# Performance work log

Hardware: AMD Instinct MI355X
Metric: run time of the kernel (lower is better)

Reference implementation:

```python
import jax, jax.numpy as jnp
import numpy as np

D_MODEL = 768
D_FF = 2048
NUM_EXPERTS = 8
TOP_K = 2


def setup_inputs() -> dict:
    key = jax.random.key(0)
    ks = jax.random.split(key, 5)
    s_in = 1.0 / np.sqrt(D_MODEL)
    s_ff = 1.0 / np.sqrt(D_FF)
    x = jax.random.normal(ks[0], (2, 1024, D_MODEL), dtype=jnp.float32)
    gate_w = jax.random.normal(ks[1], (D_MODEL, NUM_EXPERTS), dtype=jnp.float32) * s_in
    w_gate = jax.random.normal(ks[2], (NUM_EXPERTS, D_MODEL, D_FF), dtype=jnp.float32) * s_in
    w_up = jax.random.normal(ks[3], (NUM_EXPERTS, D_MODEL, D_FF), dtype=jnp.float32) * s_in
    w_down = jax.random.normal(ks[4], (NUM_EXPERTS, D_FF, D_MODEL), dtype=jnp.float32) * s_ff
    return {"x": x, "gate_w": gate_w, "w_gate": w_gate, "w_up": w_up, "w_down": w_down}


def reference(x, gate_w, w_gate, w_up, w_down):
    B, S, D = x.shape
    xf = x.reshape(-1, D)  # [T, D]

    # Router (eval mode: no noise)
    logits = xf @ gate_w                      # [T, E]
    gates = jax.nn.softmax(logits, axis=-1)
    top_g, top_i = jax.lax.top_k(gates, TOP_K)             # [T, K]
    top_g = top_g / jnp.sum(top_g, axis=-1, keepdims=True)

    # combine weights: [T, E] = sum_k gate_k * onehot(idx_k)
    combine = jnp.sum(
        jax.nn.one_hot(top_i, NUM_EXPERTS, dtype=xf.dtype) * top_g[..., None], axis=1
    )

    # SwiGLU experts computed densely, masked/weighted by combine
    g = jnp.einsum("td,edf->etf", xf, w_gate)  # [E, T, F]
    u = jnp.einsum("td,edf->etf", xf, w_up)
    h = jax.nn.silu(g) * u
    eo = jnp.einsum("etf,efd->etd", h, w_down)  # [E, T, D]
    out = jnp.einsum("te,etd->td", combine, eo)  # [T, D]

    load_balancing_loss = jnp.asarray(0.0, dtype=xf.dtype)  # eval mode
    return out.reshape(B, S, D), load_balancing_loss
```

## Files before the change

### kernel.cpp

```cpp
#include <hip/hip_runtime.h>
#include <stdint.h>

typedef __attribute__((ext_vector_type(8))) short short8;
typedef __attribute__((ext_vector_type(4))) float f32x4;
typedef unsigned int u32;
typedef unsigned short u16;

#define T_TOK 2048
#define DMODEL 768
#define DFF 2048
#define NEXP 8

#define BKP 40
#define WSTR 20

#define M_CNT 0
#define M_CUR 8
#define M_OFF 16

#define G1_GRID 640
#define G1_PERX 80
#define G2_GRID 432
#define G2_PERX 54

#define PREP_WT 9216
#define PREP_RT (PREP_WT + 512)
#define PREP_ZO (PREP_RT + 1536)

__device__ __forceinline__ float b2f(u16 u) {
  union { u32 i; float f; } v; v.i = ((u32)u) << 16; return v.f;
}
__device__ __forceinline__ u16 f2b(float f) {
  union { float f; u32 i; } v; v.f = f;
  return (u16)((v.i + 0x7fffu + ((v.i >> 16) & 1u)) >> 16);
}
__device__ __forceinline__ u32 pack2(float lo, float hi) {
  return (u32)f2b(lo) | ((u32)f2b(hi) << 16);
}
__device__ __forceinline__ uint4 cvt8(float4 a, float4 b) {
  uint4 r; r.x = pack2(a.x, a.y); r.y = pack2(a.z, a.w);
  r.z = pack2(b.x, b.y); r.w = pack2(b.z, b.w); return r;
}
__device__ __forceinline__ void gl16(const u16* g, u16* l) {
  __builtin_amdgcn_global_load_lds((const __attribute__((address_space(1))) void*)g,
                                   (__attribute__((address_space(3))) void*)l, 16, 0, 0);
}

__global__ __launch_bounds__(256) void k_prep(
    const float* __restrict__ wg, const float* __restrict__ wu, const float* __restrict__ wd,
    const float* __restrict__ x, const float* __restrict__ gw,
    u16* __restrict__ WgB, u16* __restrict__ WuB, u16* __restrict__ WdB,
    int* __restrict__ t2e, float* __restrict__ t2w, u16* __restrict__ xb,
    float* __restrict__ out) {
  __shared__ float T[32][136];
  int bid = blockIdx.x;
  int tid = threadIdx.x;
  if (bid < PREP_WT) {
    const float* in; u16* outw; int K, N, nx, ky, e, b;
    if (bid < 3072) { in = wg; outw = WgB; K = 768; N = 2048; b = bid; }
    else if (bid < 6144) { in = wu; outw = WuB; K = 768; N = 2048; b = bid - 3072; }
    else { in = wd; outw = WdB; K = 2048; N = 768; b = bid - 6144; }
    if (K == 768) {
      nx = b & 15; int r = b >> 4;
      e = (int)(((unsigned)r * 43691u) >> 20);
      ky = r - e * 24;
    } else {
      int q = (int)(((unsigned)b * 43691u) >> 18);
      nx = b - q * 6; ky = q & 63; e = q >> 6;
    }
    const float* ip = in + (size_t)e * K * N + (size_t)(ky * 32) * N + nx * 128;
    int kr = tid >> 3, nc = (tid & 7) * 16;
    const float* rp = ip + (size_t)kr * N + nc;
    float4 v0 = *(const float4*)(rp);
    float4 v1 = *(const float4*)(rp + 4);
    float4 v2 = *(const float4*)(rp + 8);
    float4 v3 = *(const float4*)(rp + 12);
    *(float4*)&T[kr][nc] = v0;
    *(float4*)&T[kr][nc + 4] = v1;
    *(float4*)&T[kr][nc + 8] = v2;
    *(float4*)&T[kr][nc + 12] = v3;
    __syncthreads();
    int nr = tid >> 1, kh = (tid & 1) * 16;
    float v[16];
#pragma unroll
    for (int j = 0; j < 16; ++j) v[j] = T[kh + j][nr];
    uint4 o0, o1;
    o0.x = pack2(v[0], v[1]);  o0.y = pack2(v[2], v[3]);
    o0.z = pack2(v[4], v[5]);  o0.w = pack2(v[6], v[7]);
    o1.x = pack2(v[8], v[9]);  o1.y = pack2(v[10], v[11]);
    o1.z = pack2(v[12], v[13]); o1.w = pack2(v[14], v[15]);
    int NB = N >> 7, KB = K >> 5;
    u16* op = outw + ((size_t)(e * NB + nx) * KB + ky) * 4096 + nr * 32 + kh;
    *(uint4*)op = o0;
    *(uint4*)(op + 8) = o1;
  } else if (bid < PREP_RT) {
    int lane = tid & 63;
    int t = (bid - PREP_WT) * 4 + (tid >> 6);
    const float* xr = x + (size_t)t * DMODEL;
    u16* xbr = xb + (size_t)t * DMODEL;
    float acc[8];
#pragma unroll
    for (int e = 0; e < 8; ++e) acc[e] = 0.f;
#pragma unroll
    for (int i = 0; i < 12; ++i) {
      int d = lane + (i << 6);
      float xd = xr[d];
      xbr[d] = f2b(xd);
      float4 g0 = *(const float4*)(gw + d * 8);
      float4 g1 = *(const float4*)(gw + d * 8 + 4);
      acc[0] += xd * g0.x; acc[1] += xd * g0.y;
      acc[2] += xd * g0.z; acc[3] += xd * g0.w;
      acc[4] += xd * g1.x; acc[5] += xd * g1.y;
      acc[6] += xd * g1.z; acc[7] += xd * g1.w;
    }
#pragma unroll
    for (int s = 32; s >= 1; s >>= 1) {
#pragma unroll
      for (int e = 0; e < 8; ++e) acc[e] += __shfl_xor(acc[e], s);
    }
    if (lane == 0) {
      int i0 = 0;
#pragma unroll
      for (int e = 1; e < 8; ++e) if (acc[e] > acc[i0]) i0 = e;
      int i1 = (i0 == 0) ? 1 : 0;
#pragma unroll
      for (int e = 0; e < 8; ++e) if (e != i0 && acc[e] > acc[i1]) i1 = e;
      float w0 = 1.f / (1.f + __expf(acc[i1] - acc[i0]));
      t2e[2 * t] = i0; t2e[2 * t + 1] = i1;
      t2w[2 * t] = w0; t2w[2 * t + 1] = 1.f - w0;
    }
  } else {
    int zid = bid - PREP_RT;
    float4 z = (float4){0.f, 0.f, 0.f, 0.f};
    *(float4*)(out + (size_t)(zid * 256 + tid) * 4) = z;
  }
}

__global__ __launch_bounds__(1024) void k_scansc(
    const int* __restrict__ t2e, const float* __restrict__ t2w, int* __restrict__ meta,
    int* __restrict__ tok_of_row, int* __restrict__ slot_of, float* __restrict__ w_of_row,
    float* __restrict__ outp) {
  __shared__ int cnt[8], cur[8];
  int tid = threadIdx.x;
  if (tid < 8) cnt[tid] = 0;
  __syncthreads();
  int e0a[2], e1a[2];
#pragma unroll
  for (int j = 0; j < 2; ++j) {
    int t = tid + j * 1024;
    e0a[j] = t2e[2 * t]; e1a[j] = t2e[2 * t + 1];
    atomicAdd(&cnt[e0a[j]], 1); atomicAdd(&cnt[e1a[j]], 1);
  }
  __syncthreads();
  if (tid == 0) {
    int r = 0;
#pragma unroll 1
    for (int e = 0; e < NEXP; ++e) {
      int c = cnt[e];
      meta[M_CNT + e] = c; meta[M_OFF + e] = r; cur[e] = r; r += c;
    }
    meta[M_OFF + NEXP] = r;
    outp[(size_t)T_TOK * DMODEL] = 0.f;
  }
  __syncthreads();
#pragma unroll
  for (int j = 0; j < 2; ++j) {
    int t = tid + j * 1024;
    int s0 = atomicAdd(&cur[e0a[j]], 1);
    tok_of_row[s0] = t; slot_of[2 * t] = s0; w_of_row[s0] = t2w[2 * t];
    int s1 = atomicAdd(&cur[e1a[j]], 1);
    tok_of_row[s1] = t; slot_of[2 * t + 1] = s1; w_of_row[s1] = t2w[2 * t + 1];
  }
}

__global__ __launch_bounds__(256, 3) void k_stage1b(
    const u16* __restrict__ Xb, const u16* __restrict__ WgB, const u16* __restrict__ WuB,
    const int* __restrict__ meta, const int* __restrict__ tok, u16* __restrict__ H) {
  __shared__ u16 Xs[2][4096];
  __shared__ u16 Wgs[2][4096];
  __shared__ u16 Wus[2][4096];
  int bid = blockIdx.x;
  int wid = (bid & 7) * G1_PERX + (bid >> 3);
  int e = 0, base = 0, Te = 0, off_e = 0, rows_e = 0;
#pragma unroll 1
  for (e = 0; e < NEXP; ++e) {
    off_e = meta[M_OFF + e];
    rows_e = meta[M_OFF + e + 1] - off_e;
    Te = (rows_e + 127) >> 7;
    int c = Te << 4;
    if (wid < base + c) break;
    base += c;
  }
  if (e == NEXP) return;
  int local = wid - base;
  int rb = local >> 4, fb = local & 15;
  int r0 = rb * 128;
  int rows_t = rows_e - r0; if (rows_t > 128) rows_t = 128;
  int f0 = fb * 128;
  int tid = threadIdx.x, lane = tid & 63, w = tid >> 6;
  int wr = w >> 1, wc = w & 1, q = lane >> 4, lm = lane & 15;

  int rsub = lane >> 2;
  int g4 = (lane & 3) ^ ((lane >> 3) & 3);
  int rA = w * 32 + rsub;
  int cA = (rA < rows_t) ? rA : (rows_t - 1);
  int cB = (rA + 16 < rows_t) ? (rA + 16) : (rows_t - 1);
  const u16* aG0 = Xb + (size_t)tok[off_e + r0 + cA] * DMODEL + g4 * 8;
  const u16* aG1 = Xb + (size_t)tok[off_e + r0 + cB] * DMODEL + g4 * 8;
  size_t cb = (size_t)((e * 16 + fb) * 24) * 4096 + w * 1024 + rsub * 32 + g4 * 8;
  const u16* gG = WgB + cb;
  const u16* uG = WuB + cb;

  int qx = (q ^ ((lm >> 1) & 3)) * 8;
  int aoff = (wr * 64 + lm) * 32 + qx;
  int boff = (wc * 64 + lm) * 32 + qx;

  f32x4 accg[4][4], accu[4][4];
#pragma unroll
  for (int i = 0; i < 4; ++i)
#pragma unroll
    for (int j = 0; j < 4; ++j) {
      accg[i][j] = (f32x4){0.f, 0.f, 0.f, 0.f};
      accu[i][j] = (f32x4){0.f, 0.f, 0.f, 0.f};
    }

  auto STG = [&](int b, int kko) {
    int ka = kko * 32;
    size_t kb = (size_t)kko * 4096;
    gl16(aG0 + ka, &Xs[b][w * 1024]);
    gl16(aG1 + ka, &Xs[b][w * 1024 + 512]);
    gl16(gG + kb, &Wgs[b][w * 1024]);
    gl16(gG + kb + 512, &Wgs[b][w * 1024 + 512]);
    gl16(uG + kb, &Wus[b][w * 1024]);
    gl16(uG + kb + 512, &Wus[b][w * 1024 + 512]);
  };
  auto CMP = [&](int b) {
    const u16* ap = &Xs[b][aoff];
    const u16* gp = &Wgs[b][boff];
    const u16* up = &Wus[b][boff];
    short8 af[4];
#pragma unroll
    for (int mt = 0; mt < 4; ++mt) af[mt] = *(const short8*)(ap + mt * 512);
#pragma unroll
    for (int nt = 0; nt < 4; ++nt) {
      short8 bg = *(const short8*)(gp + nt * 512);
      short8 bu = *(const short8*)(up + nt * 512);
#pragma unroll
      for (int mt = 0; mt < 4; ++mt) {
        accg[mt][nt] = __builtin_amdgcn_mfma_f32_16x16x32_bf16(af[mt], bg, accg[mt][nt], 0, 0, 0);
        accu[mt][nt] = __builtin_amdgcn_mfma_f32_16x16x32_bf16(af[mt], bu, accu[mt][nt], 0, 0, 0);
      }
    }
  };

  STG(0, 0);
  for (int kko = 0; kko < 23; ++kko) {
    STG((kko + 1) & 1, kko + 1);
    asm volatile("s_waitcnt vmcnt(6)" ::: "memory");
    __builtin_amdgcn_s_barrier();
    asm volatile("" ::: "memory");
    CMP(kko & 1);
    asm volatile("s_waitcnt lgkmcnt(0)" ::: "memory");
    __builtin_amdgcn_s_barrier();
    asm volatile("" ::: "memory");
  }
  asm volatile("s_waitcnt vmcnt(0)" ::: "memory");
  __builtin_amdgcn_s_barrier();
  asm volatile("" ::: "memory");
  CMP(1);

#pragma unroll
  for (int mt = 0; mt < 4; ++mt)
#pragma unroll
    for (int r = 0; r < 4; ++r) {
      int lrow = wr * 64 + mt * 16 + q * 4 + r;
      if (lrow < rows_t) {
        size_t rowbase = (size_t)(off_e + r0 + lrow) * DFF + f0 + wc * 64;
#pragma unroll
        for (int nt = 0; nt < 4; ++nt) {
          float g = accg[mt][nt][r], u = accu[mt][nt][r];
          float h = g / (1.f + __expf(-g)) * u;
          H[rowbase + nt * 16 + lm] = f2b(h);
        }
      }
    }
}

__global__ __launch_bounds__(256, 3) void k_stage2b(
    const u16* __restrict__ H, const u16* __restrict__ WdB,
    const int* __restrict__ meta, const int* __restrict__ tok,
    const float* __restrict__ wrow, float* __restrict__ out) {
  __shared__ u16 As[2][4096];
  __shared__ u16 Ws[2][8192];
  int bid = blockIdx.x;
  int wid = (bid & 7) * G2_PERX + (bid >> 3);
  int e = 0, base = 0, off_e = 0, rows_e = 0;
#pragma unroll 1
  for (e = 0; e < NEXP; ++e) {
    off_e = meta[M_OFF + e];
    rows_e = meta[M_OFF + e + 1] - off_e;
    int Tr = (rows_e + 63) >> 6;
    int c = Tr * 6;
    if (wid < base + c) break;
    base += c;
  }
  if (e == NEXP) return;
  int local = wid - base;
  int rb = (int)(((unsigned)local * 43691u) >> 18);
  int nb = local - rb * 6;
  int r0 = rb * 64;
  int rows_t = rows_e - r0; if (rows_t > 64) rows_t = 64;
  int n0 = nb * 128;
  int tid = threadIdx.x, lane = tid & 63, w = tid >> 6;
  int q = lane >> 4, lm = lane & 15;

  int rsub = lane >> 2;
  int g4 = (lane & 3) ^ ((lane >> 3) & 3);
  int rA = w * 16 + rsub;
  int cA = (rA < rows_t) ? rA : (rows_t - 1);
  const u16* aG = H + (size_t)(off_e + r0 + cA) * DFF + g4 * 8;
  size_t cb = (size_t)((e * 6 + nb) * 64) * 4096 + w * 1024 + rsub * 32 + g4 * 8;
  const u16* wG = WdB + cb;

  int qx = (q ^ ((lm >> 1) & 3)) * 8;
  int aoff = lm * 32 + qx;
  int boff = (w * 32 + lm) * 32 + qx;

  f32x4 acc[4][2];
#pragma unroll
  for (int i = 0; i < 4; ++i)
#pragma unroll
    for (int j = 0; j < 2; ++j) acc[i][j] = (f32x4){0.f, 0.f, 0.f, 0.f};

  auto STG = [&](int b, int kko) {
    int ka = kko * 64;
    size_t kb = (size_t)kko * 8192;
    gl16(aG + ka, &As[b][w * 512]);
    gl16(aG + ka + 32, &As[b][2048 + w * 512]);
    gl16(wG + kb, &Ws[b][w * 1024]);
    gl16(wG + kb + 512, &Ws[b][w * 1024 + 512]);
    gl16(wG + kb + 4096, &Ws[b][4096 + w * 1024]);
    gl16(wG + kb + 4608, &Ws[b][4096 + w * 1024 + 512]);
  };
  auto CMP = [&](int b) {
    const u16* ap = &As[b][aoff];
    const u16* bp = &Ws[b][boff];
#pragma unroll
    for (int s = 0; s < 2; ++s) {
      short8 af[4];
#pragma unroll
      for (int mt = 0; mt < 4; ++mt) af[mt] = *(const short8*)(ap + s * 2048 + mt * 512);
#pragma unroll
      for (int nt = 0; nt < 2; ++nt) {
        short8 bb = *(const short8*)(bp + s * 4096 + nt * 512);
#pragma unroll
        for (int mt = 0; mt < 4; ++mt)
          acc[mt][nt] = __builtin_amdgcn_mfma_f32_16x16x32_bf16(af[mt], bb, acc[mt][nt], 0, 0, 0);
      }
    }
  };

  STG(0, 0);
  for (int kko = 0; kko < 31; ++kko) {
    STG((kko + 1) & 1, kko + 1);
    asm volatile("s_waitcnt vmcnt(6)" ::: "memory");
    __builtin_amdgcn_s_barrier();
    asm volatile("" ::: "memory");
    CMP(kko & 1);
    asm volatile("s_waitcnt lgkmcnt(0)" ::: "memory");
    __builtin_amdgcn_s_barrier();
    asm volatile("" ::: "memory");
  }
  asm volatile("s_waitcnt vmcnt(0)" ::: "memory");
  __builtin_amdgcn_s_barrier();
  asm volatile("" ::: "memory");
  CMP(1);

#pragma unroll
  for (int mt = 0; mt < 4; ++mt)
#pragma unroll
    for (int r = 0; r < 4; ++r) {
      int lrow = mt * 16 + q * 4 + r;
      if (lrow < rows_t) {
        int row = off_e + r0 + lrow;
        int token = tok[row];
        float wgt = wrow[row];
        float* ob = out + (size_t)token * DMODEL + n0 + w * 32;
#pragma unroll
        for (int nt = 0; nt < 2; ++nt)
          atomicAdd(&ob[nt * 16 + lm], wgt * acc[mt][nt][r]);
      }
    }
}

__global__ __launch_bounds__(192) void k_combine(
    const float* __restrict__ Op, const int* __restrict__ slot_of,
    const float* __restrict__ t2w, float* __restrict__ out) {
  int t = blockIdx.x;
  int d4 = threadIdx.x << 2;
  int s0 = slot_of[2 * t], s1 = slot_of[2 * t + 1];
  float w0 = t2w[2 * t], w1 = t2w[2 * t + 1];
  float4 a = *(const float4*)&Op[(size_t)s0 * DMODEL + d4];
  float4 b = *(const float4*)&Op[(size_t)s1 * DMODEL + d4];
  float4 r;
  r.x = w0 * a.x + w1 * b.x;
  r.y = w0 * a.y + w1 * b.y;
  r.z = w0 * a.z + w1 * b.z;
  r.w = w0 * a.w + w1 * b.w;
  *(float4*)&out[(size_t)t * DMODEL + d4] = r;
}

__global__ __launch_bounds__(256) void k_router_fb(
    const float* __restrict__ x, const float* __restrict__ gw,
    int* __restrict__ t2e, float* __restrict__ t2w, u16* __restrict__ xb) {
  int lane = threadIdx.x & 63;
  int t = blockIdx.x * 4 + (threadIdx.x >> 6);
  const float* xr = x + (size_t)t * DMODEL;
  u16* xbr = xb + (size_t)t * DMODEL;
  float acc[8];
#pragma unroll
  for (int e = 0; e < 8; ++e) acc[e] = 0.f;
#pragma unroll
  for (int i = 0; i < 12; ++i) {
    int d = lane + (i << 6);
    float xd = xr[d];
    xbr[d] = f2b(xd);
    float4 g0 = *(const float4*)(gw + d * 8);
    float4 g1 = *(const float4*)(gw + d * 8 + 4);
    acc[0] += xd * g0.x; acc[1] += xd * g0.y;
    acc[2] += xd * g0.z; acc[3] += xd * g0.w;
    acc[4] += xd * g1.x; acc[5] += xd * g1.y;
    acc[6] += xd * g1.z; acc[7] += xd * g1.w;
  }
#pragma unroll
  for (int s = 32; s >= 1; s >>= 1) {
#pragma unroll
    for (int e = 0; e < 8; ++e) acc[e] += __shfl_xor(acc[e], s);
  }
  if (lane == 0) {
    int i0 = 0;
#pragma unroll
    for (int e = 1; e < 8; ++e) if (acc[e] > acc[i0]) i0 = e;
    int i1 = (i0 == 0) ? 1 : 0;
#pragma unroll
    for (int e = 0; e < 8; ++e) if (e != i0 && acc[e] > acc[i1]) i1 = e;
    float w0 = 1.f / (1.f + __expf(acc[i1] - acc[i0]));
    t2e[2 * t] = i0; t2e[2 * t + 1] = i1;
    t2w[2 * t] = w0; t2w[2 * t + 1] = 1.f - w0;
  }
}

__device__ __forceinline__ void wpack(u32* lds, int k2, int n8, uint4 a, uint4 b) {
  int idx = n8 * WSTR + k2;
  lds[idx + 0 * WSTR] = (a.x & 0xffffu) | (b.x << 16);
  lds[idx + 1 * WSTR] = (a.x >> 16) | (b.x & 0xffff0000u);
  lds[idx + 2 * WSTR] = (a.y & 0xffffu) | (b.y << 16);
  lds[idx + 3 * WSTR] = (a.y >> 16) | (b.y & 0xffff0000u);
  lds[idx + 4 * WSTR] = (a.z & 0xffffu) | (b.z << 16);
  lds[idx + 5 * WSTR] = (a.z >> 16) | (b.z & 0xffff0000u);
  lds[idx + 6 * WSTR] = (a.w & 0xffffu) | (b.w << 16);
  lds[idx + 7 * WSTR] = (a.w >> 16) | (b.w & 0xffff0000u);
}

__global__ __launch_bounds__(256) void k_stage1f(
    const float* __restrict__ xv, const float* __restrict__ wgv, const float* __restrict__ wuv,
    const int* __restrict__ meta, const int* __restrict__ tok, u16* __restrict__ H) {
  __shared__ u16 Xs[64 * 32];
  __shared__ u16 Wgs[128 * BKP];
  __shared__ u16 Wus[128 * BKP];
  int e = blockIdx.z;
  int off_e = meta[M_OFF + e];
  int rows_e = meta[M_OFF + e + 1] - off_e;
  int r0 = blockIdx.y * 64;
  if (r0 >= rows_e) return;
  int rows_t = rows_e - r0; if (rows_t > 64) rows_t = 64;
  int f0 = blockIdx.x * 128;
  int tid = threadIdx.x, lane = tid & 63, w = tid >> 6;
  int wr = w >> 1, wc = w & 1;
  int srow = (w << 4) + (lane >> 2);
  int trow = (srow < rows_t) ? tok[off_e + r0 + srow] : tok[off_e];
  int xcol = (lane & 3) << 3;
  u16* xl = &Xs[srow * 32 + xcol];
  int k2 = tid >> 4, n8 = (tid & 15) << 3;
  size_t wbase = (size_t)e * (DMODEL * DFF) + (size_t)(k2 << 1) * DFF + f0 + n8;
  f32x4 accg[2][4], accu[2][4];
#pragma unroll
  for (int i = 0; i < 2; ++i)
#pragma unroll
    for (int j = 0; j < 4; ++j) {
      accg[i][j] = (f32x4){0.f, 0.f, 0.f, 0.f};
      accu[i][j] = (f32x4){0.f, 0.f, 0.f, 0.f};
    }
  for (int kk = 0; kk < DMODEL / 32; ++kk) {
    int k0 = kk << 5;
    const float* xg = xv + (size_t)trow * DMODEL + xcol;
    const float* wgp = wgv + wbase;
    const float* wup = wuv + wbase;
    uint4 xa = cvt8(*(const float4*)(xg + k0), *(const float4*)(xg + k0 + 4));
    uint4 ga = cvt8(*(const float4*)(wgp + (size_t)k0 * DFF), *(const float4*)(wgp + (size_t)k0 * DFF + 4));
    uint4 gb = cvt8(*(const float4*)(wgp + (size_t)k0 * DFF + DFF), *(const float4*)(wgp + (size_t)k0 * DFF + DFF + 4));
    uint4 ua = cvt8(*(const float4*)(wup + (size_t)k0 * DFF), *(const float4*)(wup + (size_t)k0 * DFF + 4));
    uint4 ub = cvt8(*(const float4*)(wup + (size_t)k0 * DFF + DFF), *(const float4*)(wup + (size_t)k0 * DFF + DFF + 4));
    __syncthreads();
    *(uint4*)xl = xa;
    wpack((u32*)Wgs, k2, n8, ga, gb);
    wpack((u32*)Wus, k2, n8, ua, ub);
    __syncthreads();
    short8 af[2];
#pragma unroll
    for (int mt = 0; mt < 2; ++mt)
      af[mt] = *(const short8*)&Xs[((wr << 5) + (mt << 4) + (lane & 15)) * 32 + ((lane >> 4) << 3)];
#pragma unroll
    for (int nt = 0; nt < 4; ++nt) {
      int col = (wc << 6) + (nt << 4) + (lane & 15);
      short8 bg = *(const short8*)&Wgs[col * BKP + ((lane >> 4) << 3)];
      short8 bu = *(const short8*)&Wus[col * BKP + ((lane >> 4) << 3)];
#pragma unroll
      for (int mt = 0; mt < 2; ++mt) {
        accg[mt][nt] = __builtin_amdgcn_mfma_f32_16x16x32_bf16(af[mt], bg, accg[mt][nt], 0, 0, 0);
        accu[mt][nt] = __builtin_amdgcn_mfma_f32_16x16x32_bf16(af[mt], bu, accu[mt][nt], 0, 0, 0);
      }
    }
  }
  int q = lane >> 4, c = lane & 15;
#pragma unroll
  for (int mt = 0; mt < 2; ++mt)
#pragma unroll
    for (int r = 0; r < 4; ++r) {
      int lrow = (wr << 5) + (mt << 4) + (q << 2) + r;
      if (lrow < rows_t) {
        size_t rowbase = (size_t)(off_e + r0 + lrow) * DFF + f0 + (wc << 6);
#pragma unroll
        for (int nt = 0; nt < 4; ++nt) {
          float g = accg[mt][nt][r], u = accu[mt][nt][r];
          float h = g / (1.f + __expf(-g)) * u;
          H[rowbase + (nt << 4) + c] = f2b(h);
        }
      }
    }
}

__global__ __launch_bounds__(256) void k_stage2f(
    const u16* __restrict__ H, const float* __restrict__ wdv,
    const int* __restrict__ meta, float* __restrict__ Op) {
  __shared__ u16 As[64 * 32];
  __shared__ u16 Ws[128 * BKP];
  int e = blockIdx.z;
  int off_e = meta[M_OFF + e];
  int rows_e = meta[M_OFF + e + 1] - off_e;
  int r0 = blockIdx.y * 64;
  if (r0 >= rows_e) return;
  int rows_t = rows_e - r0; if (rows_t > 64) rows_t = 64;
  int n0 = blockIdx.x * 128;
  int tid = threadIdx.x, lane = tid & 63, w = tid >> 6;
  int wr = w >> 1, wc = w & 1;
  int srow = (w << 4) + (lane >> 2);
  int hrow = off_e + r0 + ((srow < rows_t) ? srow : 0);
  const u16* ag = H + (size_t)hrow * DFF + ((lane & 3) << 3);
  u16* al = &As[srow * 32 + ((lane & 3) << 3)];
  int k2 = tid >> 4, n8 = (tid & 15) << 3;
  size_t wbase = (size_t)e * (DFF * DMODEL) + (size_t)(k2 << 1) * DMODEL + n0 + n8;
  f32x4 acc[2][4];
#pragma unroll
  for (int i = 0; i < 2; ++i)
#pragma unroll
    for (int j = 0; j < 4; ++j) acc[i][j] = (f32x4){0.f, 0.f, 0.f, 0.f};
  for (int kk = 0; kk < DFF / 32; ++kk) {
    int k0 = kk << 5;
    uint4 xa = *(const uint4*)(ag + k0);
    const float* wdp = wdv + wbase;
    uint4 ga = cvt8(*(const float4*)(wdp + (size_t)k0 * DMODEL), *(const float4*)(wdp + (size_t)k0 * DMODEL + 4));
    uint4 gb = cvt8(*(const float4*)(wdp + (size_t)k0 * DMODEL + DMODEL), *(const float4*)(wdp + (size_t)k0 * DMODEL + DMODEL + 4));
    __syncthreads();
    *(uint4*)al = xa;
    wpack((u32*)Ws, k2, n8, ga, gb);
    __syncthreads();
    short8 af[2];
#pragma unroll
    for (int mt = 0; mt < 2; ++mt)
      af[mt] = *(const short8*)&As[((wr << 5) + (mt << 4) + (lane & 15)) * 32 + ((lane >> 4) << 3)];
#pragma unroll
    for (int nt = 0; nt < 4; ++nt) {
      int col = (wc << 6) + (nt << 4) + (lane & 15);
      short8 b = *(const short8*)&Ws[col * BKP + ((lane >> 4) << 3)];
#pragma unroll
      for (int mt = 0; mt < 2; ++mt)
        acc[mt][nt] = __builtin_amdgcn_mfma_f32_16x16x32_bf16(af[mt], b, acc[mt][nt], 0, 0, 0);
    }
  }
  int q = lane >> 4, c = lane & 15;
#pragma unroll
  for (int mt = 0; mt < 2; ++mt)
#pragma unroll
    for (int r = 0; r < 4; ++r) {
      int lrow = (wr << 5) + (mt << 4) + (q << 2) + r;
      if (lrow < rows_t) {
        size_t rowbase = (size_t)(off_e + r0 + lrow) * DMODEL + n0 + (wc << 6);
#pragma unroll
        for (int nt = 0; nt < 4; ++nt)
          Op[rowbase + (nt << 4) + c] = acc[mt][nt][r];
      }
    }
}

extern "C" void kernel_launch(void* const* d_in, const int* in_sizes, int n_in,
                              void* d_out, int out_size, void* d_ws, size_t ws_size,
                              hipStream_t stream) {
  const float* x  = (const float*)d_in[0];
  const float* gw = (const float*)d_in[1];
  const float* wg = (const float*)d_in[2];
  const float* wu = (const float*)d_in[3];
  const float* wd = (const float*)d_in[4];
  float* out = (float*)d_out;

  char* ws = (char*)d_ws;
  int* meta = (int*)ws;
  int* t2e        = (int*)(ws + 256);
  int* slot_of    = (int*)(ws + 16640);
  int* tok_of_row = (int*)(ws + 33024);
  float* t2w      = (float*)(ws + 49408);
  u16* Xb         = (u16*)(ws + 65792);

  const size_t NEED = 108069120;
  if (ws_size >= NEED) {
    u16* H         = (u16*)(ws + 3211520);
    float* w_of_row = (float*)(ws + 19988736);
    u16* WgB   = (u16*)(ws + 32571648);
    u16* WuB   = (u16*)(ws + 57737472);
    u16* WdB   = (u16*)(ws + 82903296);

    k_prep<<<PREP_ZO, 256, 0, stream>>>(wg, wu, wd, x, gw, WgB, WuB, WdB,
                                        t2e, t2w, Xb, out);
    k_scansc<<<1, 1024, 0, stream>>>(t2e, t2w, meta, tok_of_row, slot_of, w_of_row, out);
    k_stage1b<<<G1_GRID, 256, 0, stream>>>(Xb, WgB, WuB, meta, tok_of_row, H);
    k_stage2b<<<G2_GRID, 256, 0, stream>>>(H, WdB, meta, tok_of_row, w_of_row, out);
  } else {
    u16* H    = (u16*)(ws + 65792);
    float* Op = (float*)(ws + 65792 + 16777216);
    float* w_of_row = (float*)(ws + 65792 + 16777216 + 12582912);
    k_router_fb<<<T_TOK / 4, 256, 0, stream>>>(x, gw, t2e, t2w, Xb);
    k_scansc<<<1, 1024, 0, stream>>>(t2e, t2w, meta, tok_of_row, slot_of, w_of_row, out);
    dim3 g1(DFF / 128, T_TOK / 64, NEXP);
    k_stage1f<<<g1, 256, 0, stream>>>(x, wg, wu, meta, tok_of_row, H);
    dim3 g2(DMODEL / 128, T_TOK / 64, NEXP);
    k_stage2f<<<g2, 256, 0, stream>>>(H, wd, meta, Op);
    k_combine<<<T_TOK, 192, 0, stream>>>(Op, slot_of, t2w, out);
  }
}
```

Baseline: 261.9 us.

## Triple-buffer expert GEMM pipelines and batch weight conversion into fewer prep blocks

Both expert GEMM kernels move from double to triple buffering in shared memory, so two tiles stay in flight and the wait point loosens to vmcnt(12). Occupancy hints drop from 3 to 2 blocks per CU to make room for the larger LDS use. The prep kernel now converts eight k-tiles per block in a software-pipelined loop instead of launching one block per tile, and each zeroing block clears four times as much output. This cuts launch and block overhead and hides more memory latency, at the cost of occupancy and extra barriers.

```diff
diff --git a/kernel.cpp b/kernel.cpp
--- a/kernel.cpp
+++ b/kernel.cpp
@@ -23,9 +23,9 @@
 #define G2_GRID 432
 #define G2_PERX 54
 
-#define PREP_WT 9216
+#define PREP_WT 1152
 #define PREP_RT (PREP_WT + 512)
-#define PREP_ZO (PREP_RT + 1536)
+#define PREP_GRID (PREP_RT + 384)
 
 __device__ __forceinline__ float b2f(u16 u) {
   union { u32 i; float f; } v; v.i = ((u32)u) << 16; return v.f;
@@ -56,43 +56,59 @@
   int bid = blockIdx.x;
   int tid = threadIdx.x;
   if (bid < PREP_WT) {
-    const float* in; u16* outw; int K, N, nx, ky, e, b;
-    if (bid < 3072) { in = wg; outw = WgB; K = 768; N = 2048; b = bid; }
-    else if (bid < 6144) { in = wu; outw = WuB; K = 768; N = 2048; b = bid - 3072; }
-    else { in = wd; outw = WdB; K = 2048; N = 768; b = bid - 6144; }
+    const float* in; u16* outw; int K, N, b;
+    if (bid < 384) { in = wg; outw = WgB; K = 768; N = 2048; b = bid; }
+    else if (bid < 768) { in = wu; outw = WuB; K = 768; N = 2048; b = bid - 384; }
+    else { in = wd; outw = WdB; K = 2048; N = 768; b = bid - 768; }
+    int e, nx, ky0;
     if (K == 768) {
-      nx = b & 15; int r = b >> 4;
-      e = (int)(((unsigned)r * 43691u) >> 20);
-      ky = r - e * 24;
+      int t = (int)(((unsigned)b * 43691u) >> 17);
+      int kc = b - t * 3;
+      e = t >> 4; nx = t & 15; ky0 = kc * 8;
     } else {
-      int q = (int)(((unsigned)b * 43691u) >> 18);
-      nx = b - q * 6; ky = q & 63; e = q >> 6;
-    }
-    const float* ip = in + (size_t)e * K * N + (size_t)(ky * 32) * N + nx * 128;
+      int kc = b & 7; int t = b >> 3;
+      e = (int)(((unsigned)t * 43691u) >> 18);
+      nx = t - e * 6; ky0 = kc * 8;
+    }
     int kr = tid >> 3, nc = (tid & 7) * 16;
-    const float* rp = ip + (size_t)kr * N + nc;
-    float4 v0 = *(const float4*)(rp);
-    float4 v1 = *(const float4*)(rp + 4);
-    float4 v2 = *(const float4*)(rp + 8);
-    float4 v3 = *(const float4*)(rp + 12);
-    *(float4*)&T[kr][nc] = v0;
-    *(float4*)&T[kr][nc + 4] = v1;
-    *(float4*)&T[kr][nc + 8] = v2;
-    *(float4*)&T[kr][nc + 12] = v3;
-    __syncthreads();
     int nr = tid >> 1, kh = (tid & 1) * 16;
-    float v[16];
-#pragma unroll
-    for (int j = 0; j < 16; ++j) v[j] = T[kh + j][nr];
-    uint4 o0, o1;
-    o0.x = pack2(v[0], v[1]);  o0.y = pack2(v[2], v[3]);
-    o0.z = pack2(v[4], v[5]);  o0.w = pack2(v[6], v[7]);
-    o1.x = pack2(v[8], v[9]);  o1.y = pack2(v[10], v[11]);
-    o1.z = pack2(v[12], v[13]); o1.w = pack2(v[14], v[15]);
+    const float* rp = in + (size_t)e * K * N + (size_t)(ky0 * 32 + kr) * N + nx * 128 + nc;
     int NB = N >> 7, KB = K >> 5;
-    u16* op = outw + ((size_t)(e * NB + nx) * KB + ky) * 4096 + nr * 32 + kh;
-    *(uint4*)op = o0;
-    *(uint4*)(op + 8) = o1;
+    u16* op = outw + ((size_t)(e * NB + nx) * KB + ky0) * 4096 + nr * 32 + kh;
+    size_t rstep = (size_t)32 * N;
+    float4 c0 = *(const float4*)(rp);
+    float4 c1 = *(const float4*)(rp + 4);
+    float4 c2 = *(const float4*)(rp + 8);
+    float4 c3 = *(const float4*)(rp + 12);
+#pragma unroll 1
+    for (int i = 0; i < 8; ++i) {
+      float4 n0, n1, n2, n3;
+      if (i < 7) {
+        const float* np = rp + (size_t)(i + 1) * rstep;
+        n0 = *(const float4*)(np);
+        n1 = *(const float4*)(np + 4);
+        n2 = *(const float4*)(np + 8);
+        n3 = *(const float4*)(np + 12);
+      }
+      __syncthreads();
+      *(float4*)&T[kr][nc] = c0;
+      *(float4*)&T[kr][nc + 4] = c1;
+      *(float4*)&T[kr][nc + 8] = c2;
+      *(float4*)&T[kr][nc + 12] = c3;
+      __syncthreads();
+      float v[16];
+#pragma unroll
+      for (int j = 0; j < 16; ++j) v[j] = T[kh + j][nr];
+      uint4 o0, o1;
+      o0.x = pack2(v[0], v[1]);  o0.y = pack2(v[2], v[3]);
+      o0.z = pack2(v[4], v[5]);  o0.w = pack2(v[6], v[7]);
+      o1.x = pack2(v[8], v[9]);  o1.y = pack2(v[10], v[11]);
+      o1.z = pack2(v[12], v[13]); o1.w = pack2(v[14], v[15]);
+      u16* opp = op + (size_t)i * 4096;
+      *(uint4*)opp = o0;
+      *(uint4*)(opp + 8) = o1;
+      c0 = n0; c1 = n1; c2 = n2; c3 = n3;
+    }
   } else if (bid < PREP_RT) {
     int lane = tid & 63;
     int t = (bid - PREP_WT) * 4 + (tid >> 6);
@@ -132,7 +148,9 @@
   } else {
     int zid = bid - PREP_RT;
     float4 z = (float4){0.f, 0.f, 0.f, 0.f};
-    *(float4*)(out + (size_t)(zid * 256 + tid) * 4) = z;
+    float* p = out + ((size_t)zid * 256 + tid) * 16;
+    *(float4*)p = z; *(float4*)(p + 4) = z;
+    *(float4*)(p + 8) = z; *(float4*)(p + 12) = z;
   }
 }
 
@@ -173,12 +191,12 @@
   }
 }
 
-__global__ __launch_bounds__(256, 3) void k_stage1b(
+__global__ __launch_bounds__(256, 2) void k_stage1b(
     const u16* __restrict__ Xb, const u16* __restrict__ WgB, const u16* __restrict__ WuB,
     const int* __restrict__ meta, const int* __restrict__ tok, u16* __restrict__ H) {
-  __shared__ u16 Xs[2][4096];
-  __shared__ u16 Wgs[2][4096];
-  __shared__ u16 Wus[2][4096];
+  __shared__ u16 Xs[3][4096];
+  __shared__ u16 Wgs[3][4096];
+  __shared__ u16 Wus[3][4096];
   int bid = blockIdx.x;
   int wid = (bid & 7) * G1_PERX + (bid >> 3);
   int e = 0, base = 0, Te = 0, off_e = 0, rows_e = 0;
@@ -253,21 +271,29 @@
     }
   };
 
-  STG(0, 0);
-  for (int kko = 0; kko < 23; ++kko) {
-    STG((kko + 1) & 1, kko + 1);
-    asm volatile("s_waitcnt vmcnt(6)" ::: "memory");
+  STG(0, 0); STG(1, 1);
+  int cur = 0, nxt = 2;
+#pragma unroll 1
+  for (int kko = 0; kko < 22; ++kko) {
+    STG(nxt, kko + 2);
+    asm volatile("s_waitcnt vmcnt(12)" ::: "memory");
     __builtin_amdgcn_s_barrier();
     asm volatile("" ::: "memory");
-    CMP(kko & 1);
+    CMP(cur);
     asm volatile("s_waitcnt lgkmcnt(0)" ::: "memory");
     __builtin_amdgcn_s_barrier();
     asm volatile("" ::: "memory");
-  }
+    cur = (cur == 2) ? 0 : cur + 1;
+    nxt = (nxt == 2) ? 0 : nxt + 1;
+  }
+  asm volatile("s_waitcnt vmcnt(6)" ::: "memory");
+  __builtin_amdgcn_s_barrier();
+  asm volatile("" ::: "memory");
+  CMP(1);
   asm volatile("s_waitcnt vmcnt(0)" ::: "memory");
   __builtin_amdgcn_s_barrier();
   asm volatile("" ::: "memory");
-  CMP(1);
+  CMP(2);
 
 #pragma unroll
   for (int mt = 0; mt < 4; ++mt)
@@ -286,12 +312,12 @@
     }
 }
 
-__global__ __launch_bounds__(256, 3) void k_stage2b(
+__global__ __launch_bounds__(256, 2) void k_stage2b(
     const u16* __restrict__ H, const u16* __restrict__ WdB,
     const int* __restrict__ meta, const int* __restrict__ tok,
     const float* __restrict__ wrow, float* __restrict__ out) {
-  __shared__ u16 As[2][4096];
-  __shared__ u16 Ws[2][8192];
+  __shared__ u16 As[3][4096];
+  __shared__ u16 Ws[3][8192];
   int bid = blockIdx.x;
   int wid = (bid & 7) * G2_PERX + (bid >> 3);
   int e = 0, base = 0, off_e = 0, rows_e = 0;
@@ -360,17 +386,25 @@
     }
   };
 
-  STG(0, 0);
-  for (int kko = 0; kko < 31; ++kko) {
-    STG((kko + 1) & 1, kko + 1);
-    asm volatile("s_waitcnt vmcnt(6)" ::: "memory");
+  STG(0, 0); STG(1, 1);
+  int cur = 0, nxt = 2;
+#pragma unroll 1
+  for (int kko = 0; kko < 30; ++kko) {
+    STG(nxt, kko + 2);
+    asm volatile("s_waitcnt vmcnt(12)" ::: "memory");
     __builtin_amdgcn_s_barrier();
     asm volatile("" ::: "memory");
-    CMP(kko & 1);
+    CMP(cur);
     asm volatile("s_waitcnt lgkmcnt(0)" ::: "memory");
     __builtin_amdgcn_s_barrier();
     asm volatile("" ::: "memory");
-  }
+    cur = (cur == 2) ? 0 : cur + 1;
+    nxt = (nxt == 2) ? 0 : nxt + 1;
+  }
+  asm volatile("s_waitcnt vmcnt(6)" ::: "memory");
+  __builtin_amdgcn_s_barrier();
+  asm volatile("" ::: "memory");
+  CMP(0);
   asm volatile("s_waitcnt vmcnt(0)" ::: "memory");
   __builtin_amdgcn_s_barrier();
   asm volatile("" ::: "memory");
@@ -629,8 +663,8 @@
     u16* WuB   = (u16*)(ws + 57737472);
     u16* WdB   = (u16*)(ws + 82903296);
 
-    k_prep<<<PREP_ZO, 256, 0, stream>>>(wg, wu, wd, x, gw, WgB, WuB, WdB,
-                                        t2e, t2w, Xb, out);
+    k_prep<<<PREP_GRID, 256, 0, stream>>>(wg, wu, wd, x, gw, WgB, WuB, WdB,
+                                          t2e, t2w, Xb, out);
     k_scansc<<<1, 1024, 0, stream>>>(t2e, t2w, meta, tok_of_row, slot_of, w_of_row, out);
     k_stage1b<<<G1_GRID, 256, 0, stream>>>(Xb, WgB, WuB, meta, tok_of_row, H);
     k_stage2b<<<G2_GRID, 256, 0, stream>>>(H, WdB, meta, tok_of_row, w_of_row, out);
```

New measurement: 278.5 us. +6.3%, slower.

## Move down-projection weight conversion into stage-1 grid to overlap with GEMM

Applied to the files above, without the earlier changes.

The w_down fp32-to-bf16 transpose/convert blocks move out of the prep kernel and are appended as extra blocks of the stage-1 GEMM launch, so that conversion can run alongside the gate/up GEMM tiles instead of delaying routing and stage 1. Stage-1 shared memory becomes one raw char buffer reused by both block types. The output zeroing now writes 16 floats per thread with fewer blocks. The cost is extra scheduled blocks in stage 1 that compete for CUs, and block ordering means the conversion blocks may simply run after the GEMM tiles.

```diff
diff --git a/kernel.cpp b/kernel.cpp
--- a/kernel.cpp
+++ b/kernel.cpp
@@ -22,10 +22,11 @@
 #define G1_PERX 80
 #define G2_GRID 432
 #define G2_PERX 54
-
-#define PREP_WT 9216
+#define S1_GRID (G1_GRID + 3072)
+
+#define PREP_WT 6144
 #define PREP_RT (PREP_WT + 512)
-#define PREP_ZO (PREP_RT + 1536)
+#define PREP_GRID (PREP_RT + 384)
 
 __device__ __forceinline__ float b2f(u16 u) {
   union { u32 i; float f; } v; v.i = ((u32)u) << 16; return v.f;
@@ -47,30 +48,24 @@
 }
 
 __global__ __launch_bounds__(256) void k_prep(
-    const float* __restrict__ wg, const float* __restrict__ wu, const float* __restrict__ wd,
+    const float* __restrict__ wg, const float* __restrict__ wu,
     const float* __restrict__ x, const float* __restrict__ gw,
-    u16* __restrict__ WgB, u16* __restrict__ WuB, u16* __restrict__ WdB,
+    u16* __restrict__ WgB, u16* __restrict__ WuB,
     int* __restrict__ t2e, float* __restrict__ t2w, u16* __restrict__ xb,
     float* __restrict__ out) {
   __shared__ float T[32][136];
   int bid = blockIdx.x;
   int tid = threadIdx.x;
   if (bid < PREP_WT) {
-    const float* in; u16* outw; int K, N, nx, ky, e, b;
-    if (bid < 3072) { in = wg; outw = WgB; K = 768; N = 2048; b = bid; }
-    else if (bid < 6144) { in = wu; outw = WuB; K = 768; N = 2048; b = bid - 3072; }
-    else { in = wd; outw = WdB; K = 2048; N = 768; b = bid - 6144; }
-    if (K == 768) {
-      nx = b & 15; int r = b >> 4;
-      e = (int)(((unsigned)r * 43691u) >> 20);
-      ky = r - e * 24;
-    } else {
-      int q = (int)(((unsigned)b * 43691u) >> 18);
-      nx = b - q * 6; ky = q & 63; e = q >> 6;
-    }
-    const float* ip = in + (size_t)e * K * N + (size_t)(ky * 32) * N + nx * 128;
+    const float* in; u16* outw; int b;
+    if (bid < 3072) { in = wg; outw = WgB; b = bid; }
+    else { in = wu; outw = WuB; b = bid - 3072; }
+    int nx = b & 15; int r = b >> 4;
+    int e = (int)(((unsigned)r * 43691u) >> 20);
+    int ky = r - e * 24;
+    const float* ip = in + (size_t)e * (768 * 2048) + (size_t)(ky * 32) * 2048 + nx * 128;
     int kr = tid >> 3, nc = (tid & 7) * 16;
-    const float* rp = ip + (size_t)kr * N + nc;
+    const float* rp = ip + (size_t)kr * 2048 + nc;
     float4 v0 = *(const float4*)(rp);
     float4 v1 = *(const float4*)(rp + 4);
     float4 v2 = *(const float4*)(rp + 8);
@@ -89,8 +84,7 @@
     o0.z = pack2(v[4], v[5]);  o0.w = pack2(v[6], v[7]);
     o1.x = pack2(v[8], v[9]);  o1.y = pack2(v[10], v[11]);
     o1.z = pack2(v[12], v[13]); o1.w = pack2(v[14], v[15]);
-    int NB = N >> 7, KB = K >> 5;
-    u16* op = outw + ((size_t)(e * NB + nx) * KB + ky) * 4096 + nr * 32 + kh;
+    u16* op = outw + ((size_t)(e * 16 + nx) * 24 + ky) * 4096 + nr * 32 + kh;
     *(uint4*)op = o0;
     *(uint4*)(op + 8) = o1;
   } else if (bid < PREP_RT) {
@@ -132,7 +126,9 @@
   } else {
     int zid = bid - PREP_RT;
     float4 z = (float4){0.f, 0.f, 0.f, 0.f};
-    *(float4*)(out + (size_t)(zid * 256 + tid) * 4) = z;
+    float* p = out + ((size_t)zid * 256 + tid) * 16;
+    *(float4*)p = z; *(float4*)(p + 4) = z;
+    *(float4*)(p + 8) = z; *(float4*)(p + 12) = z;
   }
 }
 
@@ -175,11 +171,45 @@
 
 __global__ __launch_bounds__(256, 3) void k_stage1b(
     const u16* __restrict__ Xb, const u16* __restrict__ WgB, const u16* __restrict__ WuB,
-    const int* __restrict__ meta, const int* __restrict__ tok, u16* __restrict__ H) {
-  __shared__ u16 Xs[2][4096];
-  __shared__ u16 Wgs[2][4096];
-  __shared__ u16 Wus[2][4096];
+    const int* __restrict__ meta, const int* __restrict__ tok, u16* __restrict__ H,
+    const float* __restrict__ wd, u16* __restrict__ WdB) {
+  __shared__ __align__(16) char smem[49152];
   int bid = blockIdx.x;
+  int tid = threadIdx.x;
+  if (bid >= G1_GRID) {
+    float (*T)[136] = (float(*)[136])smem;
+    int b = bid - G1_GRID;
+    int qq = (int)(((unsigned)b * 43691u) >> 18);
+    int nx = b - qq * 6, ky = qq & 63, e = qq >> 6;
+    const float* ip = wd + (size_t)e * (2048 * 768) + (size_t)(ky * 32) * 768 + nx * 128;
+    int kr = tid >> 3, nc = (tid & 7) * 16;
+    const float* rp = ip + (size_t)kr * 768 + nc;
+    float4 v0 = *(const float4*)(rp);
+    float4 v1 = *(const float4*)(rp + 4);
+    float4 v2 = *(const float4*)(rp + 8);
+    float4 v3 = *(const float4*)(rp + 12);
+    *(float4*)&T[kr][nc] = v0;
+    *(float4*)&T[kr][nc + 4] = v1;
+    *(float4*)&T[kr][nc + 8] = v2;
+    *(float4*)&T[kr][nc + 12] = v3;
+    __syncthreads();
+    int nr = tid >> 1, kh = (tid & 1) * 16;
+    float v[16];
+#pragma unroll
+    for (int j = 0; j < 16; ++j) v[j] = T[kh + j][nr];
+    uint4 o0, o1;
+    o0.x = pack2(v[0], v[1]);  o0.y = pack2(v[2], v[3]);
+    o0.z = pack2(v[4], v[5]);  o0.w = pack2(v[6], v[7]);
+    o1.x = pack2(v[8], v[9]);  o1.y = pack2(v[10], v[11]);
+    o1.z = pack2(v[12], v[13]); o1.w = pack2(v[14], v[15]);
+    u16* op = WdB + ((size_t)(e * 6 + nx) * 64 + ky) * 4096 + nr * 32 + kh;
+    *(uint4*)op = o0;
+    *(uint4*)(op + 8) = o1;
+    return;
+  }
+  u16* XsB  = (u16*)smem;
+  u16* WgsB = (u16*)(smem + 16384);
+  u16* WusB = (u16*)(smem + 32768);
   int wid = (bid & 7) * G1_PERX + (bid >> 3);
   int e = 0, base = 0, Te = 0, off_e = 0, rows_e = 0;
 #pragma unroll 1
@@ -197,7 +227,7 @@
   int r0 = rb * 128;
   int rows_t = rows_e - r0; if (rows_t > 128) rows_t = 128;
   int f0 = fb * 128;
-  int tid = threadIdx.x, lane = tid & 63, w = tid >> 6;
+  int lane = tid & 63, w = tid >> 6;
   int wr = w >> 1, wc = w & 1, q = lane >> 4, lm = lane & 15;
 
   int rsub = lane >> 2;
@@ -227,17 +257,17 @@
   auto STG = [&](int b, int kko) {
     int ka = kko * 32;
     size_t kb = (size_t)kko * 4096;
-    gl16(aG0 + ka, &Xs[b][w * 1024]);
-    gl16(aG1 + ka, &Xs[b][w * 1024 + 512]);
-    gl16(gG + kb, &Wgs[b][w * 1024]);
-    gl16(gG + kb + 512, &Wgs[b][w * 1024 + 512]);
-    gl16(uG + kb, &Wus[b][w * 1024]);
-    gl16(uG + kb + 512, &Wus[b][w * 1024 + 512]);
+    gl16(aG0 + ka, XsB + b * 4096 + w * 1024);
+    gl16(aG1 + ka, XsB + b * 4096 + w * 1024 + 512);
+    gl16(gG + kb, WgsB + b * 4096 + w * 1024);
+    gl16(gG + kb + 512, WgsB + b * 4096 + w * 1024 + 512);
+    gl16(uG + kb, WusB + b * 4096 + w * 1024);
+    gl16(uG + kb + 512, WusB + b * 4096 + w * 1024 + 512);
   };
   auto CMP = [&](int b) {
-    const u16* ap = &Xs[b][aoff];
-    const u16* gp = &Wgs[b][boff];
-    const u16* up = &Wus[b][boff];
+    const u16* ap = XsB + b * 4096 + aoff;
+    const u16* gp = WgsB + b * 4096 + boff;
+    const u16* up = WusB + b * 4096 + boff;
     short8 af[4];
 #pragma unroll
     for (int mt = 0; mt < 4; ++mt) af[mt] = *(const short8*)(ap + mt * 512);
@@ -629,10 +659,10 @@
     u16* WuB   = (u16*)(ws + 57737472);
     u16* WdB   = (u16*)(ws + 82903296);
 
-    k_prep<<<PREP_ZO, 256, 0, stream>>>(wg, wu, wd, x, gw, WgB, WuB, WdB,
-                                        t2e, t2w, Xb, out);
+    k_prep<<<PREP_GRID, 256, 0, stream>>>(wg, wu, x, gw, WgB, WuB,
+                                          t2e, t2w, Xb, out);
     k_scansc<<<1, 1024, 0, stream>>>(t2e, t2w, meta, tok_of_row, slot_of, w_of_row, out);
-    k_stage1b<<<G1_GRID, 256, 0, stream>>>(Xb, WgB, WuB, meta, tok_of_row, H);
+    k_stage1b<<<S1_GRID, 256, 0, stream>>>(Xb, WgB, WuB, meta, tok_of_row, H, wd, WdB);
     k_stage2b<<<G2_GRID, 256, 0, stream>>>(H, WdB, meta, tok_of_row, w_of_row, out);
   } else {
     u16* H    = (u16*)(ws + 65792);
```

Result: faster. 254.9 us (-2.6%).
